# Optimization experiments

Hardware: AMD Instinct MI355X
Metric: run time of the kernel (lower is better)

The kernel has to match this reference:

```python
import jax, jax.numpy as jnp
import numpy as np

B, T, D, H, W = 2, 16, 64, 64, 64
MAX_GROWTH = 0.0  # max_growth_rate init kwarg

def _ln(x, g, b):
    m = x.mean(-1, keepdims=True)
    v = x.var(-1, keepdims=True)
    return (x - m) * jax.lax.rsqrt(v + 1e-5) * g + b

def _pscan(A, X):
    # linear recurrence h_t = A_t*h_{t-1} + X_t via Blelchlo-style associative scan over axis 1
    def comb(l, r):
        a1, x1 = l
        a2, x2 = r
        return a1 * a2, a2 * x1 + x2
    return jax.lax.associative_scan(comb, (A, X), axis=1)[1]

def setup_inputs() -> dict:
    key = jax.random.key(0)
    ks = jax.random.split(key, 20)
    n = lambda k, s, sc=1.0: jax.random.normal(k, s, dtype=jnp.float32) * sc
    inp = dict(
        x_re=n(ks[0], (B, T, D, H, W)), x_im=n(ks[1], (B, T, D, H, W)),
        h_re=n(ks[2], (B * H * W, 1, D)), h_im=n(ks[3], (B * H * W, 1, D)),
        flux_re=n(ks[4], (B, D)), flux_im=n(ks[5], (B, D)),
        dt_seq=0.01 + 0.1 * jax.random.uniform(ks[6], (B, T), dtype=jnp.float32),
        g_s=jnp.ones(2 * D, jnp.float32), b_s=jnp.zeros(2 * D, jnp.float32),
        Wc=n(ks[7], (3, 3, 2 * D, 2 * D), 1.0 / np.sqrt(9 * 2 * D)), bc=jnp.zeros(2 * D, jnp.float32),
        g_t=jnp.ones(2 * D, jnp.float32), b_t=jnp.zeros(2 * D, jnp.float32),
        E_re=n(ks[8], (D, D), 1.0 / np.sqrt(D)), E_im=n(ks[9], (D, D), 1.0 / np.sqrt(D)),
        Dec_re=n(ks[10], (D, D), 1.0 / np.sqrt(D)), Dec_im=n(ks[11], (D, D), 1.0 / np.sqrt(D)),
        lam_flux_raw=jnp.zeros(D, jnp.float32),
        Wsrc_re=n(ks[12], (D, D), 1.0 / np.sqrt(D)), Wsrc_im=n(ks[13], (D, D), 1.0 / np.sqrt(D)),
        w_gate=n(ks[14], (D,)), b_gate=jnp.zeros(D, jnp.float32),
        lam_re_raw=jnp.ones(D, jnp.float32), lam_im=n(ks[15], (D,)),
        W1=n(ks[16], (2 * D, 8 * D), 1.0 / np.sqrt(2 * D)), b1=jnp.zeros(8 * D, jnp.float32),
        W2=n(ks[17], (8 * D, 2 * D), 1.0 / np.sqrt(8 * D)), b2=jnp.zeros(2 * D, jnp.float32),
    )
    return inp

def _forward(x_re, x_im, h_re, h_im, flux_re, flux_im, dt_seq, g_s, b_s, Wc, bc, g_t, b_t,
             E_re, E_im, Dec_re, Dec_im, lam_flux_raw, Wsrc_re, Wsrc_im, w_gate, b_gate,
             lam_re_raw, lam_im, W1, b1, W2, b2):
    # channel-last complex field (B,T,H,W,D)
    x = jnp.moveaxis(x_re, 2, -1) + 1j * jnp.moveaxis(x_im, 2, -1)
    # --- spatial residual branch: LN -> Clifford(= real 2D conv on [re;im] channels) ---
    xr = jnp.concatenate([x.real, x.imag], -1)  # (B,T,H,W,2D)
    xn = _ln(xr, g_s, b_s).reshape(B * T, H, W, 2 * D)
    xs = jax.lax.conv_general_dilated(xn, Wc, (1, 1), 'SAME',
                                      dimension_numbers=('NHWC', 'HWIO', 'NHWC')) + bc
    xs = xs.reshape(B, T, H, W, 2 * D)
    x = x + (xs[..., :D] + 1j * xs[..., D:])
    # --- eigen-basis encode ---
    x_eig = jnp.einsum('bthwd,de->bthwe', x, E_re + 1j * E_im)
    x_mean = x_eig.mean((2, 3))  # (B,T,D)
    # --- flux tracker scan ---
    lam_f = jax.nn.softplus(lam_flux_raw)
    A_flux = jnp.exp(-lam_f * dt_seq[..., None])  # (B,T,D) real decay
    flux = _pscan(A_flux.astype(x_mean.dtype), x_mean * dt_seq[..., None])
    flux = flux + (flux_re + 1j * flux_im)[:, None, :] * jnp.cumprod(A_flux, axis=1)
    source = jnp.einsum('btd,de->bte', flux, Wsrc_re + 1j * Wsrc_im)
    gate = jax.nn.sigmoid(flux.real * w_gate + b_gate)  # real gate in [0,1]
    flux_out = flux[:, -1]
    ge = gate[:, :, None, None, :]
    forcing = x_eig * ge + source[:, :, None, None, :] * (1.0 - ge)
    # --- temporal propagator (exact exponential integrator) ---
    lam = (MAX_GROWTH - jax.nn.softplus(lam_re_raw)) + 1j * lam_im  # Re(lam) <= max_growth_rate
    op_decay = jnp.exp(lam * dt_seq[..., None])            # (B,T,D)
    op_forcing = (op_decay - 1.0) / lam
    u = forcing * op_forcing[:, :, None, None, :]          # (B,T,H,W,D)
    h_prev = (h_re + 1j * h_im).reshape(B, H, W, D)
    u = u.at[:, 0].add(h_prev * op_decay[:, 0][:, None, None, :])
    A_full = jnp.broadcast_to(op_decay[:, :, None, None, :], u.shape)
    u_out = _pscan(A_full, u)                              # (B,T,H,W,D)
    h_out = u_out[:, -1].reshape(B * H * W, 1, D)
    # --- decode + temporal LN/FFN residual ---
    decoded = jnp.einsum('bthwd,de->bthwe', u_out, Dec_re + 1j * Dec_im)
    dn = _ln(jnp.concatenate([decoded.real, decoded.imag], -1), g_t, b_t)
    h1 = jax.nn.gelu(jnp.einsum('bthwc,cf->bthwf', dn, W1) + b1)
    d2 = jnp.einsum('bthwf,fc->bthwc', h1, W2) + b2
    delta = d2[..., :D] + 1j * d2[..., D:]
    z = x + decoded + delta
    return z, h_out, flux_out

def reference(x_re, x_im, h_re, h_im, flux_re, flux_im, dt_seq, g_s, b_s, Wc, bc, g_t, b_t,
              E_re, E_im, Dec_re, Dec_im, lam_flux_raw, Wsrc_re, Wsrc_im, w_gate, b_gate,
              lam_re_raw, lam_im, W1, b1, W2, b2):
    z, h_out, flux_out = _forward(x_re, x_im, h_re, h_im, flux_re, flux_im, dt_seq, g_s, b_s,
                                  Wc, bc, g_t, b_t, E_re, E_im, Dec_re, Dec_im, lam_flux_raw,
                                  Wsrc_re, Wsrc_im, w_gate, b_gate, lam_re_raw, lam_im,
                                  W1, b1, W2, b2)
    # complex outputs returned as real/imag stacked on last axis
    return (jnp.stack([z.real, z.imag], -1),
            jnp.stack([h_out.real, h_out.imag], -1),
            jnp.stack([flux_out.real, flux_out.imag], -1))
```

## Files before the change

### kernel.cpp

```cpp
#include <hip/hip_runtime.h>
#include <hip/hip_bf16.h>


typedef __hip_bfloat16 bf16;
typedef __attribute__((ext_vector_type(8))) short bhalf8;
typedef __attribute__((ext_vector_type(4))) float floatx4;

#define DEV __device__ __forceinline__

DEV float b2f(const bf16 x) { return __bfloat162float(x); }
DEV bf16  f2b(float x)      { return __float2bfloat16(x); }
DEV unsigned short f2bu(float x) { bf16 h = f2b(x); return *(unsigned short*)&h; }
DEV float bu2f(unsigned short u) { unsigned int t = ((unsigned int)u) << 16; return *(float*)&t; }
DEV float softplusf(float x){ return x > 20.f ? x : log1pf(expf(x)); }
DEV float geluf(float x) {
    float v = x * fmaf(x * x, 0.0713548162726f, 1.5957691216057308f);
    float e = __expf(-v);
    return x * __builtin_amdgcn_rcpf(1.f + e);
}

static constexpr int B_ = 2, T_ = 16, D_ = 64, HW = 4096;
static constexpr int NPIX = B_ * T_ * HW;
static constexpr long long N1 = (long long)NPIX * 128;

static constexpr long long BUFA  = 0;
static constexpr long long XUBF  = N1;
static constexpr long long DECBF = N1 + N1 / 2;
static constexpr long long XNBF  = 2 * N1;
static constexpr long long XCBF  = 2 * N1 + N1 / 2;
static constexpr long long XMEAN = 3 * N1;
static constexpr long long TABS  = XMEAN + 4096;
static constexpr long long FLAGO = TABS + 14336;
static constexpr long long WCP   = FLAGO + 64;
static constexpr long long W1P   = WCP + 73728;
static constexpr long long W2P   = W1P + 32768;
static constexpr long long WEP   = W2P + 32768;
static constexpr long long WDP   = WEP + 8192;

static constexpr long long ZOUT = 0;
static constexpr long long HOUT = 16777216;
static constexpr long long FOUT = 17825792;

DEV float ld(const void* p, long long i, bool bf) {
    if (bf) return b2f(((const bf16*)p)[i]);
    return ((const float*)p)[i];
}

__global__ void k_detect(const unsigned short* __restrict__ x, float* __restrict__ ws) {
    int lane = threadIdx.x;
    int cnt = 0;
    for (int i = lane; i < 256; i += 64) {
        int e = (x[i] >> 7) & 0xFF;
        cnt += (e >= 100 && e <= 140) ? 1 : 0;
    }
    for (int m = 1; m < 64; m <<= 1) cnt += __shfl_xor(cnt, m, 64);
    if (lane == 0) ws[FLAGO] = (cnt >= 224) ? 1.f : 0.f;
}

__global__ void k_convert(const void* Wc, const void* W1, const void* W2,
                          const void* Er, const void* Ei, const void* Dr, const void* Di,
                          float* ws) {
    bool bf = ws[FLAGO] != 0.f;
    int i = blockIdx.x * 256 + threadIdx.x;
    unsigned short* wcp = (unsigned short*)(ws + WCP);
    unsigned short* w1p = (unsigned short*)(ws + W1P);
    unsigned short* w2p = (unsigned short*)(ws + W2P);
    unsigned short* wep = (unsigned short*)(ws + WEP);
    unsigned short* wdp = (unsigned short*)(ws + WDP);
    if (i < 147456) {
        int j = i & 7, lane = (i >> 3) & 63, nt = (i >> 9) & 7, kc = (i >> 12) & 3, tap = i >> 14;
        int ic = kc * 32 + ((lane >> 4) << 3) + j, oc = nt * 16 + (lane & 15);
        wcp[i] = f2bu(ld(Wc, tap * 16384 + ic * 128 + oc, bf)); return;
    } i -= 147456;
    if (i < 65536) {
        int j = i & 7, lane = (i >> 3) & 63, nt = (i >> 9) & 31, kc = i >> 14;
        int ic = kc * 32 + ((lane >> 4) << 3) + j, oc = nt * 16 + (lane & 15);
        w1p[i] = f2bu(ld(W1, ic * 512 + oc, bf)); return;
    } i -= 65536;
    if (i < 65536) {
        int j = i & 7, lane = (i >> 3) & 63, nt = (i >> 9) & 7, kc = i >> 12;
        int ic = kc * 32 + ((lane >> 4) << 3) + j, oc = nt * 16 + (lane & 15);
        w2p[i] = f2bu(ld(W2, ic * 128 + oc, bf)); return;
    } i -= 65536;
    if (i < 16384) {
        int j = i & 7, lane = (i >> 3) & 63, nt = (i >> 9) & 7, kc = i >> 12;
        int k = kc * 32 + ((lane >> 4) << 3) + j, n = nt * 16 + (lane & 15);
        float v;
        if (k < 64) v = (n < 64) ? ld(Er, k * 64 + n, bf) : ld(Ei, k * 64 + (n - 64), bf);
        else        v = (n < 64) ? -ld(Ei, (k - 64) * 64 + n, bf) : ld(Er, (k - 64) * 64 + (n - 64), bf);
        wep[i] = f2bu(v); return;
    } i -= 16384;
    if (i < 16384) {
        int j = i & 7, lane = (i >> 3) & 63, nt = (i >> 9) & 7, kc = i >> 12;
        int k = kc * 32 + ((lane >> 4) << 3) + j, n = nt * 16 + (lane & 15);
        float v;
        if (k < 64) v = (n < 64) ? ld(Dr, k * 64 + n, bf) : ld(Di, k * 64 + (n - 64), bf);
        else        v = (n < 64) ? -ld(Di, (k - 64) * 64 + n, bf) : ld(Dr, (k - 64) * 64 + (n - 64), bf);
        wdp[i] = f2bu(v); return;
    }
}

__global__ __launch_bounds__(256) void kA_ln(const void* __restrict__ xre,
                                             const void* __restrict__ xim,
                                             const void* __restrict__ gs,
                                             const void* __restrict__ bs,
                                             float* __restrict__ ws) {
    __shared__ unsigned short sr[64][72] __attribute__((aligned(16)));
    __shared__ unsigned short si[64][72] __attribute__((aligned(16)));
    __shared__ float red[2][4][64];
    __shared__ float mv[64], rv[64], gb[256];
    bool bf = ws[FLAGO] != 0.f;
    int blk = blockIdx.x;
    int bt = blk >> 6;
    int px0 = (blk & 63) * 64;
    int tid = threadIdx.x;
    gb[tid] = (tid < 128) ? ld(gs, tid, bf) : ld(bs, tid - 128, bf);
    if (bf) {
        const unsigned short* xr16 = (const unsigned short*)xre;
        const unsigned short* xi16 = (const unsigned short*)xim;
        for (int l = tid; l < 1024; l += 256) {
            int a = l >> 9, dd = (l >> 3) & 63, ck = l & 7;
            long long src = (long long)bt * 262144 + (long long)dd * 4096 + px0 + ck * 8;
            bhalf8 v = *(const bhalf8*)&(a ? xi16 : xr16)[src];
            *(bhalf8*)&(a ? si : sr)[dd][ck * 8] = v;
        }
    } else {
        for (int l = tid; l < 8192; l += 256) {
            int a = l >> 12, dd = (l >> 6) & 63, px = l & 63;
            float v = ((const float*)(a ? xim : xre))[(long long)bt * 262144 + (long long)dd * 4096 + px0 + px];
            (a ? si : sr)[dd][px] = f2bu(v);
        }
    }
    __syncthreads();
    int px = tid & 63, part = tid >> 6;
    float s = 0.f, ss = 0.f;
    for (int d = part * 16; d < part * 16 + 16; d++) {
        float r = bu2f(sr[d][px]), q = bu2f(si[d][px]);
        s += r + q; ss += r * r + q * q;
    }
    red[0][part][px] = s; red[1][part][px] = ss;
    __syncthreads();
    if (tid < 64) {
        float S  = red[0][0][tid] + red[0][1][tid] + red[0][2][tid] + red[0][3][tid];
        float SS = red[1][0][tid] + red[1][1][tid] + red[1][2][tid] + red[1][3][tid];
        float m = S * (1.f / 128.f);
        mv[tid] = m;
        rv[tid] = rsqrtf(SS * (1.f / 128.f) - m * m + 1e-5f);
    }
    __syncthreads();
    unsigned short* xcb = (unsigned short*)(ws + XCBF);
    unsigned short* xnb = (unsigned short*)(ws + XNBF);
    long long pbase = ((long long)bt * 4096 + px0) * 128;
    for (int l = tid; l < 8192; l += 256) {
        int p2 = l >> 7, ch = l & 127, d = ch & 63;
        unsigned short raw = (ch < 64 ? sr : si)[d][p2];
        float v = bu2f(raw);
        xcb[pbase + p2 * 128 + ch] = raw;
        xnb[pbase + p2 * 128 + ch] = f2bu((v - mv[p2]) * rv[p2] * gb[ch] + gb[128 + ch]);
    }
}

__global__ __launch_bounds__(256) void kB_conv(const void* __restrict__ bc,
                                               float* __restrict__ ws) {
    __shared__ unsigned short xt[3][64][136] __attribute__((aligned(16)));
    bool bf = ws[FLAGO] != 0.f;
    int blk = blockIdx.x, bt = blk >> 6, h = blk & 63;
    int tid = threadIdx.x, lane = tid & 63, wv = tid >> 6;
    int m16 = lane & 15, quad = lane >> 4;
    const unsigned short* xnb = (const unsigned short*)(ws + XNBF);
    const unsigned short* wcp = (const unsigned short*)(ws + WCP);
    bhalf8 zero8 = {0, 0, 0, 0, 0, 0, 0, 0};
    for (int l = tid; l < 3072; l += 256) {
        int r = l >> 10, rem = l & 1023, col = rem >> 4, ck = rem & 15;
        int hr = h - 1 + r;
        bhalf8 v = zero8;
        if (hr >= 0 && hr < 64)
            v = *(const bhalf8*)&xnb[(((long long)bt * 4096 + hr * 64 + col) << 7) + ck * 8];
        *(bhalf8*)&xt[r][col][ck * 8] = v;
    }
    __syncthreads();
    floatx4 acc[4][2];
    #pragma unroll
    for (int mt = 0; mt < 4; mt++)
        #pragma unroll
        for (int nt = 0; nt < 2; nt++)
            acc[mt][nt] = (floatx4){0.f, 0.f, 0.f, 0.f};
    for (int tap = 0; tap < 9; tap++) {
        int dy = tap / 3, dx = tap - dy * 3;
        #pragma unroll
        for (int kc = 0; kc < 4; kc++) {
            bhalf8 bfr[2];
            #pragma unroll
            for (int nt = 0; nt < 2; nt++)
                bfr[nt] = *(const bhalf8*)&wcp[((((tap * 4 + kc) * 8) + (wv * 2 + nt)) * 64 + lane) * 8];
            #pragma unroll
            for (int mt = 0; mt < 4; mt++) {
                int col = mt * 16 + m16 + dx - 1;
                bhalf8 af = zero8;
                if (col >= 0 && col < 64)
                    af = *(const bhalf8*)&xt[dy][col][kc * 32 + quad * 8];
                acc[mt][0] = __builtin_amdgcn_mfma_f32_16x16x32_bf16(af, bfr[0], acc[mt][0], 0, 0, 0);
                acc[mt][1] = __builtin_amdgcn_mfma_f32_16x16x32_bf16(af, bfr[1], acc[mt][1], 0, 0, 0);
            }
        }
    }
    const unsigned short* xcb = (const unsigned short*)(ws + XCBF);
    unsigned short* xub = (unsigned short*)(ws + XUBF);
    #pragma unroll
    for (int nt = 0; nt < 2; nt++) {
        int n = wv * 32 + nt * 16 + m16;
        float bcv = ld(bc, n, bf);
        #pragma unroll
        for (int mt = 0; mt < 4; mt++)
            #pragma unroll
            for (int r = 0; r < 4; r++) {
                int m = mt * 16 + quad * 4 + r;
                long long p = (long long)bt * 4096 + h * 64 + m;
                xub[p * 128 + n] = f2bu(acc[mt][nt][r] + bu2f(xcb[p * 128 + n]) + bcv);
            }
    }
}

__global__ __launch_bounds__(256) void kC_eig(float* __restrict__ ws) {
    __shared__ unsigned short At[64][136] __attribute__((aligned(16)));
    int blk = blockIdx.x, bt = blk >> 6;
    long long px0 = (long long)blk * 64;
    int tid = threadIdx.x, lane = tid & 63, wv = tid >> 6;
    int m16 = lane & 15, quad = lane >> 4;
    const unsigned short* xub = (const unsigned short*)(ws + XUBF);
    for (int l = tid; l < 1024; l += 256) {
        int p2 = l >> 4, ck = l & 15;
        *(bhalf8*)&At[p2][ck * 8] = *(const bhalf8*)&xub[(px0 + p2) * 128 + ck * 8];
    }
    __syncthreads();
    const unsigned short* wep = (const unsigned short*)(ws + WEP);
    floatx4 acc[4][2];
    #pragma unroll
    for (int mt = 0; mt < 4; mt++)
        #pragma unroll
        for (int nt = 0; nt < 2; nt++)
            acc[mt][nt] = (floatx4){0.f, 0.f, 0.f, 0.f};
    #pragma unroll
    for (int kc = 0; kc < 4; kc++) {
        bhalf8 bfr[2];
        #pragma unroll
        for (int nt = 0; nt < 2; nt++)
            bfr[nt] = *(const bhalf8*)&wep[(((kc * 8) + wv * 2 + nt) * 64 + lane) * 8];
        #pragma unroll
        for (int mt = 0; mt < 4; mt++) {
            bhalf8 af = *(const bhalf8*)&At[mt * 16 + m16][kc * 32 + quad * 8];
            acc[mt][0] = __builtin_amdgcn_mfma_f32_16x16x32_bf16(af, bfr[0], acc[mt][0], 0, 0, 0);
            acc[mt][1] = __builtin_amdgcn_mfma_f32_16x16x32_bf16(af, bfr[1], acc[mt][1], 0, 0, 0);
        }
    }
    unsigned short* xeb = (unsigned short*)(ws + BUFA);
    #pragma unroll
    for (int nt = 0; nt < 2; nt++) {
        int n = wv * 32 + nt * 16 + m16;
        float part = 0.f;
        #pragma unroll
        for (int mt = 0; mt < 4; mt++)
            #pragma unroll
            for (int r = 0; r < 4; r++) {
                int m = mt * 16 + quad * 4 + r;
                xeb[(px0 + m) * 128 + n] = f2bu(acc[mt][nt][r]);
                part += acc[mt][nt][r];
            }
        part += __shfl_xor(part, 16, 64);
        part += __shfl_xor(part, 32, 64);
        if (quad == 0) atomicAdd(ws + XMEAN + bt * 128 + n, part);
    }
}

__global__ __launch_bounds__(256) void kD_flux(const void* __restrict__ fxr, const void* __restrict__ fxi,
                                               const void* __restrict__ dtseq, const void* __restrict__ lamflux,
                                               const void* __restrict__ Wsr, const void* __restrict__ Wsi,
                                               const void* __restrict__ wgate, const void* __restrict__ bgate,
                                               const void* __restrict__ lamreraw, const void* __restrict__ lamim,
                                               float* __restrict__ ws, void* __restrict__ outv) {
    bool bfo = ws[FLAGO] != 0.f;
    int b = blockIdx.x;
    int tid = threadIdx.x;
    int d = tid & 63, g = tid >> 6;
    __shared__ float fr[64], fi[64], psr[4][64], psi[4][64];
    float lam_f = softplusf(ld(lamflux, d, bfo));
    float lre = -softplusf(ld(lamreraw, d, bfo));
    float lim = ld(lamim, d, bfo);
    float cr = 0.f, ci = 0.f;
    if (g == 0) { cr = ld(fxr, b * 64 + d, bfo); ci = ld(fxi, b * 64 + d, bfo); }
    float* tabs = ws + TABS;
    const float* xmean = ws + XMEAN;
    for (int t = 0; t < 16; t++) {
        float dt = ld(dtseq, b * 16 + t, bfo);
        int idx = b * 1024 + t * 64 + d;
        if (g == 0) {
            float A = expf(-lam_f * dt);
            float xr = xmean[(b * 16 + t) * 128 + d]      * (1.f / 4096.f) * dt;
            float xq = xmean[(b * 16 + t) * 128 + 64 + d] * (1.f / 4096.f) * dt;
            cr = A * cr + xr; ci = A * ci + xq;
            fr[d] = cr; fi[d] = ci;
        }
        __syncthreads();
        {
            float pr = 0.f, pi = 0.f;
            #pragma unroll
            for (int k = 0; k < 16; k++) {
                int d2 = g * 16 + k;
                float wr = ld(Wsr, d2 * 64 + d, bfo), wi = ld(Wsi, d2 * 64 + d, bfo);
                pr += fr[d2] * wr - fi[d2] * wi;
                pi += fr[d2] * wi + fi[d2] * wr;
            }
            psr[g][d] = pr; psi[g][d] = pi;
        }
        if (g == 1) {
            float od  = expf(lre * dt);
            float odr = od * cosf(lim * dt);
            float odi = od * sinf(lim * dt);
            tabs[3 * 2048 + idx] = odr; tabs[4 * 2048 + idx] = odi;
            float den = lre * lre + lim * lim;
            float tr = odr - 1.f;
            tabs[5 * 2048 + idx] = (tr * lre + odi * lim) / den;
            tabs[6 * 2048 + idx] = (odi * lre - tr * lim) / den;
        }
        __syncthreads();
        if (g == 0) {
            float sr = psr[0][d] + psr[1][d] + psr[2][d] + psr[3][d];
            float si2 = psi[0][d] + psi[1][d] + psi[2][d] + psi[3][d];
            tabs[1 * 2048 + idx] = sr; tabs[2 * 2048 + idx] = si2;
            tabs[0 * 2048 + idx] = 1.f / (1.f + expf(-(cr * ld(wgate, d, bfo) + ld(bgate, d, bfo))));
            if (t == 15) {
                if (bfo) {
                    bf16* ob = (bf16*)outv;
                    ob[FOUT + (b * 64 + d) * 2]     = f2b(cr);
                    ob[FOUT + (b * 64 + d) * 2 + 1] = f2b(ci);
                } else {
                    float* of = (float*)outv;
                    of[FOUT + (b * 64 + d) * 2]     = cr;
                    of[FOUT + (b * 64 + d) * 2 + 1] = ci;
                }
            }
        }
    }
}

__global__ __launch_bounds__(256) void kE_scan(const void* __restrict__ hre,
                                               const void* __restrict__ him,
                                               float* __restrict__ ws, void* __restrict__ outv) {
    __shared__ float tab[7][16][64];
    bool bfo = ws[FLAGO] != 0.f;
    long long G = (long long)blockIdx.x * 256 + threadIdx.x;
    int d = threadIdx.x & 63;
    int pix = (int)((G >> 6) & 4095);
    int b = (int)(G >> 18);
    const float* tabs = ws + TABS;
    for (int l = threadIdx.x; l < 7 * 1024; l += 256) {
        int a = l >> 10, idx = l & 1023;
        ((float*)tab)[l] = tabs[a * 2048 + b * 1024 + idx];
    }
    __syncthreads();
    long long hidx = ((long long)b * 4096 + pix) * 64 + d;
    float cr = ld(hre, hidx, bfo), ci = ld(him, hidx, bfo);
    const unsigned short* xe = (const unsigned short*)(ws + BUFA);
    unsigned short* ub = (unsigned short*)(ws + XCBF);
    for (int t = 0; t < 16; t++) {
        long long base = ((long long)((b * 16 + t) * 4096 + pix)) * 128 + d;
        float xr = bu2f(xe[base]), xi = bu2f(xe[base + 64]);
        float gt = tab[0][t][d], sr = tab[1][t][d], si = tab[2][t][d];
        float odr = tab[3][t][d], odi = tab[4][t][d];
        float ofr = tab[5][t][d], ofi = tab[6][t][d];
        float fre = xr * gt + sr * (1.f - gt);
        float fim = xi * gt + si * (1.f - gt);
        float ure = fre * ofr - fim * ofi;
        float uim = fre * ofi + fim * ofr;
        float ncr = odr * cr - odi * ci + ure;
        float nci = odr * ci + odi * cr + uim;
        cr = ncr; ci = nci;
        ub[base] = f2bu(cr); ub[base + 64] = f2bu(ci);
    }
    if (bfo) {
        __hip_bfloat162 hv; hv.x = f2b(cr); hv.y = f2b(ci);
        ((__hip_bfloat162*)((bf16*)outv + HOUT))[hidx] = hv;
    } else {
        float2 hv; hv.x = cr; hv.y = ci;
        ((float2*)((float*)outv + HOUT))[hidx] = hv;
    }
}

__global__ __launch_bounds__(256) void kF1_dec(const void* __restrict__ gt_,
                                               const void* __restrict__ bt_,
                                               float* __restrict__ ws) {
    __shared__ unsigned short At[64][136] __attribute__((aligned(16)));
    __shared__ float Ct[64][132];
    __shared__ float mv[64], rv[64], gbt[256];
    bool bf = ws[FLAGO] != 0.f;
    long long px0 = (long long)blockIdx.x * 64;
    int tid = threadIdx.x, lane = tid & 63, wv = tid >> 6;
    int m16 = lane & 15, quad = lane >> 4;
    gbt[tid] = (tid < 128) ? ld(gt_, tid, bf) : ld(bt_, tid - 128, bf);
    const unsigned short* uo = (const unsigned short*)(ws + XCBF);
    for (int l = tid; l < 1024; l += 256) {
        int p2 = l >> 4, ck = l & 15;
        *(bhalf8*)&At[p2][ck * 8] = *(const bhalf8*)&uo[(px0 + p2) * 128 + ck * 8];
    }
    __syncthreads();
    const unsigned short* wdp = (const unsigned short*)(ws + WDP);
    floatx4 acc[4][2];
    #pragma unroll
    for (int mt = 0; mt < 4; mt++)
        #pragma unroll
        for (int nt = 0; nt < 2; nt++)
            acc[mt][nt] = (floatx4){0.f, 0.f, 0.f, 0.f};
    #pragma unroll
    for (int kc = 0; kc < 4; kc++) {
        bhalf8 bfr[2];
        #pragma unroll
        for (int nt = 0; nt < 2; nt++)
            bfr[nt] = *(const bhalf8*)&wdp[(((kc * 8) + wv * 2 + nt) * 64 + lane) * 8];
        #pragma unroll
        for (int mt = 0; mt < 4; mt++) {
            bhalf8 af = *(const bhalf8*)&At[mt * 16 + m16][kc * 32 + quad * 8];
            acc[mt][0] = __builtin_amdgcn_mfma_f32_16x16x32_bf16(af, bfr[0], acc[mt][0], 0, 0, 0);
            acc[mt][1] = __builtin_amdgcn_mfma_f32_16x16x32_bf16(af, bfr[1], acc[mt][1], 0, 0, 0);
        }
    }
    #pragma unroll
    for (int nt = 0; nt < 2; nt++) {
        int n = wv * 32 + nt * 16 + m16;
        #pragma unroll
        for (int mt = 0; mt < 4; mt++)
            #pragma unroll
            for (int r = 0; r < 4; r++)
                Ct[mt * 16 + quad * 4 + r][n] = acc[mt][nt][r];
    }
    __syncthreads();
    if (tid < 64) {
        float s = 0.f, ss = 0.f;
        for (int ch = 0; ch < 128; ch++) { float v = Ct[tid][ch]; s += v; ss += v * v; }
        float m = s * (1.f / 128.f);
        mv[tid] = m;
        rv[tid] = rsqrtf(ss * (1.f / 128.f) - m * m + 1e-5f);
    }
    __syncthreads();
    unsigned short* decb = (unsigned short*)(ws + DECBF);
    unsigned short* dnb  = (unsigned short*)(ws + XNBF);
    for (int l = tid; l < 8192; l += 256) {
        int p2 = l >> 7, ch = l & 127;
        float v = Ct[p2][ch];
        decb[(px0 + p2) * 128 + ch] = f2bu(v);
        dnb [(px0 + p2) * 128 + ch] = f2bu((v - mv[p2]) * rv[p2] * gbt[ch] + gbt[128 + ch]);
    }
}

__global__ __launch_bounds__(256) void kMLP(const void* __restrict__ b1v,
                                            const void* __restrict__ b2v,
                                            float* __restrict__ ws, void* __restrict__ outv) {
    __shared__ unsigned short A1[32][136] __attribute__((aligned(16)));
    __shared__ unsigned short h1[32][520] __attribute__((aligned(16)));
    __shared__ float gb2[128];
    bool bf = ws[FLAGO] != 0.f;
    long long px0 = (long long)blockIdx.x * 32;
    int tid = threadIdx.x, lane = tid & 63, wv = tid >> 6;
    int m16 = lane & 15, quad = lane >> 4;
    const unsigned short* dnb = (const unsigned short*)(ws + XNBF);
    if (tid < 128) gb2[tid] = ld(b2v, tid, bf);
    for (int l = tid; l < 512; l += 256) {
        int p2 = l >> 4, ck = l & 15;
        *(bhalf8*)&A1[p2][ck * 8] = *(const bhalf8*)&dnb[(px0 + p2) * 128 + ck * 8];
    }
    __syncthreads();
    const unsigned short* w1p = (const unsigned short*)(ws + W1P);
    floatx4 acc1[2][8];
    #pragma unroll
    for (int mt = 0; mt < 2; mt++)
        #pragma unroll
        for (int nt = 0; nt < 8; nt++)
            acc1[mt][nt] = (floatx4){0.f, 0.f, 0.f, 0.f};
    #pragma unroll
    for (int kc = 0; kc < 4; kc++) {
        bhalf8 af0 = *(const bhalf8*)&A1[m16][kc * 32 + quad * 8];
        bhalf8 af1 = *(const bhalf8*)&A1[16 + m16][kc * 32 + quad * 8];
        #pragma unroll
        for (int nt = 0; nt < 8; nt++) {
            bhalf8 bfr = *(const bhalf8*)&w1p[(((kc * 32) + wv * 8 + nt) * 64 + lane) * 8];
            acc1[0][nt] = __builtin_amdgcn_mfma_f32_16x16x32_bf16(af0, bfr, acc1[0][nt], 0, 0, 0);
            acc1[1][nt] = __builtin_amdgcn_mfma_f32_16x16x32_bf16(af1, bfr, acc1[1][nt], 0, 0, 0);
        }
    }
    #pragma unroll
    for (int nt = 0; nt < 8; nt++) {
        int n = (wv * 8 + nt) * 16 + m16;
        float b1f = ld(b1v, n, bf);
        #pragma unroll
        for (int mt = 0; mt < 2; mt++)
            #pragma unroll
            for (int r = 0; r < 4; r++)
                h1[mt * 16 + quad * 4 + r][n] = f2bu(geluf(acc1[mt][nt][r] + b1f));
    }
    __syncthreads();
    const unsigned short* w2p = (const unsigned short*)(ws + W2P);
    floatx4 acc2[2][2];
    #pragma unroll
    for (int mt = 0; mt < 2; mt++)
        #pragma unroll
        for (int nt = 0; nt < 2; nt++)
            acc2[mt][nt] = (floatx4){0.f, 0.f, 0.f, 0.f};
    for (int kc = 0; kc < 16; kc++) {
        bhalf8 af0 = *(const bhalf8*)&h1[m16][kc * 32 + quad * 8];
        bhalf8 af1 = *(const bhalf8*)&h1[16 + m16][kc * 32 + quad * 8];
        #pragma unroll
        for (int nt = 0; nt < 2; nt++) {
            bhalf8 bfr = *(const bhalf8*)&w2p[(((kc * 8) + wv * 2 + nt) * 64 + lane) * 8];
            acc2[0][nt] = __builtin_amdgcn_mfma_f32_16x16x32_bf16(af0, bfr, acc2[0][nt], 0, 0, 0);
            acc2[1][nt] = __builtin_amdgcn_mfma_f32_16x16x32_bf16(af1, bfr, acc2[1][nt], 0, 0, 0);
        }
    }
    __syncthreads();
    #pragma unroll
    for (int nt = 0; nt < 2; nt++) {
        int n = wv * 32 + nt * 16 + m16;
        #pragma unroll
        for (int mt = 0; mt < 2; mt++)
            #pragma unroll
            for (int r = 0; r < 4; r++)
                A1[mt * 16 + quad * 4 + r][n] = f2bu(acc2[mt][nt][r]);
    }
    __syncthreads();
    {
        const unsigned short* decb = (const unsigned short*)(ws + DECBF);
        const unsigned short* xub  = (const unsigned short*)(ws + XUBF);
        int pxl = tid >> 3, dc = (tid & 7) * 8;
        long long p = px0 + pxl;
        bhalf8 cre = *(const bhalf8*)&A1[pxl][dc];
        bhalf8 cim = *(const bhalf8*)&A1[pxl][64 + dc];
        bhalf8 xr8 = *(const bhalf8*)&xub[p * 128 + dc];
        bhalf8 xi8 = *(const bhalf8*)&xub[p * 128 + 64 + dc];
        bhalf8 dr8 = *(const bhalf8*)&decb[p * 128 + dc];
        bhalf8 di8 = *(const bhalf8*)&decb[p * 128 + 64 + dc];
        float zr[8], zi[8];
        #pragma unroll
        for (int k = 0; k < 8; k++) {
            zr[k] = bu2f((unsigned short)cre[k]) + gb2[dc + k]
                  + bu2f((unsigned short)xr8[k]) + bu2f((unsigned short)dr8[k]);
            zi[k] = bu2f((unsigned short)cim[k]) + gb2[64 + dc + k]
                  + bu2f((unsigned short)xi8[k]) + bu2f((unsigned short)di8[k]);
        }
        if (bf) {
            unsigned short o[16];
            #pragma unroll
            for (int k = 0; k < 8; k++) { o[2 * k] = f2bu(zr[k]); o[2 * k + 1] = f2bu(zi[k]); }
            unsigned short* ob = (unsigned short*)outv;
            *(bhalf8*)&ob[ZOUT + p * 128 + 2 * dc]     = *(bhalf8*)&o[0];
            *(bhalf8*)&ob[ZOUT + p * 128 + 2 * dc + 8] = *(bhalf8*)&o[8];
        } else {
            float* of = (float*)outv + ZOUT + p * 128 + 2 * dc;
            #pragma unroll
            for (int k = 0; k < 8; k++) { of[2 * k] = zr[k]; of[2 * k + 1] = zi[k]; }
        }
    }
}

extern "C" void kernel_launch(void* const* d_in, const int* in_sizes, int n_in,
                              void* d_out, int out_size, void* d_ws, size_t ws_size,
                              hipStream_t stream) {
    const void* x_re  = d_in[0];
    const void* x_im  = d_in[1];
    const void* h_re  = d_in[2];
    const void* h_im  = d_in[3];
    const void* fl_re = d_in[4];
    const void* fl_im = d_in[5];
    const void* dtseq = d_in[6];
    const void* g_s   = d_in[7];
    const void* b_s   = d_in[8];
    const void* Wc    = d_in[9];
    const void* bc    = d_in[10];
    const void* g_t   = d_in[11];
    const void* b_t   = d_in[12];
    const void* E_re  = d_in[13];
    const void* E_im  = d_in[14];
    const void* De_re = d_in[15];
    const void* De_im = d_in[16];
    const void* lamfl = d_in[17];
    const void* Ws_re = d_in[18];
    const void* Ws_im = d_in[19];
    const void* wgate = d_in[20];
    const void* bgate = d_in[21];
    const void* lamrr = d_in[22];
    const void* lamim = d_in[23];
    const void* W1    = d_in[24];
    const void* b1    = d_in[25];
    const void* W2    = d_in[26];
    const void* b2    = d_in[27];
    float* ws = (float*)d_ws;

    hipMemsetAsync((char*)d_ws + XMEAN * sizeof(float), 0, 4096 * sizeof(float), stream);
    k_detect<<<1, 64, 0, stream>>>((const unsigned short*)x_re, ws);
    k_convert<<<1216, 256, 0, stream>>>(Wc, W1, W2, E_re, E_im, De_re, De_im, ws);
    kA_ln<<<2048, 256, 0, stream>>>(x_re, x_im, g_s, b_s, ws);
    kB_conv<<<2048, 256, 0, stream>>>(bc, ws);
    kC_eig<<<2048, 256, 0, stream>>>(ws);
    kD_flux<<<2, 256, 0, stream>>>(fl_re, fl_im, dtseq, lamfl, Ws_re, Ws_im,
                                   wgate, bgate, lamrr, lamim, ws, d_out);
    kE_scan<<<2048, 256, 0, stream>>>(h_re, h_im, ws, d_out);
    kF1_dec<<<2048, 256, 0, stream>>>(g_t, b_t, ws);
    kMLP<<<4096, 256, 0, stream>>>(b1, b2, ws, d_out);
}
```

Before: 454.2 us.

## Split MLP hidden layer into two phases with fragment-ordered LDS tile

The kMLP kernel now computes the 512-wide hidden layer in two halves, each feeding the second GEMM right away. This halves the live first-GEMM accumulators and shrinks the hidden-activation LDS buffer into an MFMA-fragment-ordered layout read with one vector load per lane. A launch-bounds minimum of 5 blocks per CU is added, and GELU now uses exp2 with prescaled constants. The aim is higher occupancy and fewer LDS bank conflicts, at the cost of an extra barrier per phase and possible register spills under the tighter bound.

```diff
diff --git a/kernel.cpp b/kernel.cpp
--- a/kernel.cpp
+++ b/kernel.cpp
@@ -14,8 +14,8 @@
 DEV float bu2f(unsigned short u) { unsigned int t = ((unsigned int)u) << 16; return *(float*)&t; }
 DEV float softplusf(float x){ return x > 20.f ? x : log1pf(expf(x)); }
 DEV float geluf(float x) {
-    float v = x * fmaf(x * x, 0.0713548162726f, 1.5957691216057308f);
-    float e = __expf(-v);
+    float v = x * fmaf(x * x, 0.10294324f, 2.30220819f);
+    float e = __builtin_amdgcn_exp2f(-v);
     return x * __builtin_amdgcn_rcpf(1.f + e);
 }
 
@@ -451,11 +451,11 @@
     }
 }
 
-__global__ __launch_bounds__(256) void kMLP(const void* __restrict__ b1v,
-                                            const void* __restrict__ b2v,
-                                            float* __restrict__ ws, void* __restrict__ outv) {
+__global__ __launch_bounds__(256, 5) void kMLP(const void* __restrict__ b1v,
+                                               const void* __restrict__ b2v,
+                                               float* __restrict__ ws, void* __restrict__ outv) {
     __shared__ unsigned short A1[32][136] __attribute__((aligned(16)));
-    __shared__ unsigned short h1[32][520] __attribute__((aligned(16)));
+    __shared__ unsigned short h1f[8][2][64][8] __attribute__((aligned(16)));
     __shared__ float gb2[128];
     bool bf = ws[FLAGO] != 0.f;
     long long px0 = (long long)blockIdx.x * 32;
@@ -469,34 +469,6 @@
     }
     __syncthreads();
     const unsigned short* w1p = (const unsigned short*)(ws + W1P);
-    floatx4 acc1[2][8];
-    #pragma unroll
-    for (int mt = 0; mt < 2; mt++)
-        #pragma unroll
-        for (int nt = 0; nt < 8; nt++)
-            acc1[mt][nt] = (floatx4){0.f, 0.f, 0.f, 0.f};
-    #pragma unroll
-    for (int kc = 0; kc < 4; kc++) {
-        bhalf8 af0 = *(const bhalf8*)&A1[m16][kc * 32 + quad * 8];
-        bhalf8 af1 = *(const bhalf8*)&A1[16 + m16][kc * 32 + quad * 8];
-        #pragma unroll
-        for (int nt = 0; nt < 8; nt++) {
-            bhalf8 bfr = *(const bhalf8*)&w1p[(((kc * 32) + wv * 8 + nt) * 64 + lane) * 8];
-            acc1[0][nt] = __builtin_amdgcn_mfma_f32_16x16x32_bf16(af0, bfr, acc1[0][nt], 0, 0, 0);
-            acc1[1][nt] = __builtin_amdgcn_mfma_f32_16x16x32_bf16(af1, bfr, acc1[1][nt], 0, 0, 0);
-        }
-    }
-    #pragma unroll
-    for (int nt = 0; nt < 8; nt++) {
-        int n = (wv * 8 + nt) * 16 + m16;
-        float b1f = ld(b1v, n, bf);
-        #pragma unroll
-        for (int mt = 0; mt < 2; mt++)
-            #pragma unroll
-            for (int r = 0; r < 4; r++)
-                h1[mt * 16 + quad * 4 + r][n] = f2bu(geluf(acc1[mt][nt][r] + b1f));
-    }
-    __syncthreads();
     const unsigned short* w2p = (const unsigned short*)(ws + W2P);
     floatx4 acc2[2][2];
     #pragma unroll
@@ -504,17 +476,57 @@
         #pragma unroll
         for (int nt = 0; nt < 2; nt++)
             acc2[mt][nt] = (floatx4){0.f, 0.f, 0.f, 0.f};
-    for (int kc = 0; kc < 16; kc++) {
-        bhalf8 af0 = *(const bhalf8*)&h1[m16][kc * 32 + quad * 8];
-        bhalf8 af1 = *(const bhalf8*)&h1[16 + m16][kc * 32 + quad * 8];
-        #pragma unroll
-        for (int nt = 0; nt < 2; nt++) {
-            bhalf8 bfr = *(const bhalf8*)&w2p[(((kc * 8) + wv * 2 + nt) * 64 + lane) * 8];
-            acc2[0][nt] = __builtin_amdgcn_mfma_f32_16x16x32_bf16(af0, bfr, acc2[0][nt], 0, 0, 0);
-            acc2[1][nt] = __builtin_amdgcn_mfma_f32_16x16x32_bf16(af1, bfr, acc2[1][nt], 0, 0, 0);
-        }
-    }
-    __syncthreads();
+
+    #pragma unroll
+    for (int ph = 0; ph < 2; ph++) {
+        floatx4 acc1[2][4];
+        #pragma unroll
+        for (int mt = 0; mt < 2; mt++)
+            #pragma unroll
+            for (int nt4 = 0; nt4 < 4; nt4++)
+                acc1[mt][nt4] = (floatx4){0.f, 0.f, 0.f, 0.f};
+        #pragma unroll
+        for (int kc = 0; kc < 4; kc++) {
+            bhalf8 af0 = *(const bhalf8*)&A1[m16][kc * 32 + quad * 8];
+            bhalf8 af1 = *(const bhalf8*)&A1[16 + m16][kc * 32 + quad * 8];
+            #pragma unroll
+            for (int nt4 = 0; nt4 < 4; nt4++) {
+                int nt = ph * 4 + nt4;
+                bhalf8 bfr = *(const bhalf8*)&w1p[(((kc * 32) + wv * 8 + nt) * 64 + lane) * 8];
+                acc1[0][nt4] = __builtin_amdgcn_mfma_f32_16x16x32_bf16(af0, bfr, acc1[0][nt4], 0, 0, 0);
+                acc1[1][nt4] = __builtin_amdgcn_mfma_f32_16x16x32_bf16(af1, bfr, acc1[1][nt4], 0, 0, 0);
+            }
+        }
+        #pragma unroll
+        for (int nt4 = 0; nt4 < 4; nt4++) {
+            int nt = ph * 4 + nt4;
+            int n = (wv * 8 + nt) * 16 + m16;
+            float b1f = ld(b1v, n, bf);
+            int qp = ((nt * 2) + (m16 >> 3)) & 3;
+            int slot = wv * 2 + (nt4 >> 1);
+            int j = m16 & 7;
+            #pragma unroll
+            for (int mt = 0; mt < 2; mt++)
+                #pragma unroll
+                for (int r = 0; r < 4; r++)
+                    h1f[slot][mt][qp * 16 + quad * 4 + r][j] =
+                        f2bu(geluf(acc1[mt][nt4][r] + b1f));
+        }
+        __syncthreads();
+        #pragma unroll
+        for (int s = 0; s < 8; s++) {
+            int kc2g = (s >> 1) * 4 + (s & 1) + ph * 2;
+            bhalf8 a0 = *(const bhalf8*)&h1f[s][0][lane][0];
+            bhalf8 a1 = *(const bhalf8*)&h1f[s][1][lane][0];
+            #pragma unroll
+            for (int nt = 0; nt < 2; nt++) {
+                bhalf8 bfr = *(const bhalf8*)&w2p[(((kc2g * 8) + wv * 2 + nt) * 64 + lane) * 8];
+                acc2[0][nt] = __builtin_amdgcn_mfma_f32_16x16x32_bf16(a0, bfr, acc2[0][nt], 0, 0, 0);
+                acc2[1][nt] = __builtin_amdgcn_mfma_f32_16x16x32_bf16(a1, bfr, acc2[1][nt], 0, 0, 0);
+            }
+        }
+        if (ph == 0) __syncthreads();
+    }
     #pragma unroll
     for (int nt = 0; nt < 2; nt++) {
         int n = wv * 32 + nt * 16 + m16;
```

Result: no change. 450.3 us (-0.9%).
